# Kernel tuning notes

Hardware: AMD Instinct MI355X
Metric: run time of the kernel (lower is better)

Reference implementation:

```python
import jax, jax.numpy as jnp
import numpy as np

B, S, D_IN, D_OUT = 4, 2048, 1024, 1024


def setup_inputs() -> dict:
    key = jax.random.key(0)
    k1, k2, k3, k4 = jax.random.split(key, 4)
    scale = 1.0 / np.sqrt(D_IN)
    return {
        "x": jax.random.normal(k1, (B, S, D_IN), dtype=jnp.float32),
        # torch nn.Linear weights have shape [d_out, d_in]
        "Wq": jax.random.normal(k2, (D_OUT, D_IN), dtype=jnp.float32) * scale,
        "Wk": jax.random.normal(k3, (D_OUT, D_IN), dtype=jnp.float32) * scale,
        "Wv": jax.random.normal(k4, (D_OUT, D_IN), dtype=jnp.float32) * scale,
    }


def reference(x, Wq, Wk, Wv):
    # Linear projections (torch Linear: y = x @ W.T), no bias
    q = jnp.einsum('bsd,od->bso', x, Wq)
    k = jnp.einsum('bsd,od->bso', x, Wk)
    v = jnp.einsum('bsd,od->bso', x, Wv)
    s = q.shape[1]
    scores = jnp.einsum('bqd,bkd->bqk', q, k)  # [B, S, S]
    causal = jnp.tril(jnp.ones((s, s), dtype=bool))  # True = keep
    scores = jnp.where(causal[None], scores, -jnp.inf)
    scale = jnp.asarray(k.shape[-1], scores.dtype) ** 0.5
    weights = jax.nn.softmax(scores / scale, axis=-1)
    return jnp.einsum('bqk,bkd->bqd', weights, v)
```

## Files before the change

kernel.cpp:

```cpp
#include <hip/hip_runtime.h>

#define BATCH 4
#define SEQ   2048
#define DIM   1024
#define MTOT  (BATCH * SEQ)
#define BK    32

typedef __bf16 bf16x8 __attribute__((ext_vector_type(8)));
typedef float  f32x4  __attribute__((ext_vector_type(4)));

__device__ __forceinline__ void gl_lds16(const __bf16* g, __bf16* l) {
    __builtin_amdgcn_global_load_lds(
        (const __attribute__((address_space(1))) void*)g,
        (__attribute__((address_space(3))) void*)l,
        16, 0, 0);
}

__global__ __launch_bounds__(256) void zerol_kernel(float* __restrict__ l)
{
    l[blockIdx.x * 256 + threadIdx.x] = 0.f;
}

__global__ __launch_bounds__(256) void cvt_all_kernel(
    const float* __restrict__ x,  const float* __restrict__ w0,
    const float* __restrict__ w1, const float* __restrict__ w2,
    __bf16* __restrict__ xd, __bf16* __restrict__ d0,
    __bf16* __restrict__ d1, __bf16* __restrict__ d2)
{
    const int bid = blockIdx.x;
    const float* s;
    __bf16* d;
    int base;
    if (bid < 4096)      { s = x;  d = xd; base = bid; }
    else if (bid < 4608) { s = w0; d = d0; base = bid - 4096; }
    else if (bid < 5120) { s = w1; d = d1; base = bid - 4608; }
    else                 { s = w2; d = d2; base = bid - 5120; }
    const int i = (base * 256 + threadIdx.x) * 8;
    const float4 a = *(const float4*)(s + i);
    const float4 b = *(const float4*)(s + i + 4);
    bf16x8 o;
    o[0] = (__bf16)a.x; o[1] = (__bf16)a.y; o[2] = (__bf16)a.z; o[3] = (__bf16)a.w;
    o[4] = (__bf16)b.x; o[5] = (__bf16)b.y; o[6] = (__bf16)b.z; o[7] = (__bf16)b.w;
    *(bf16x8*)(d + i) = o;
}

__device__ __forceinline__ void gemm_core(
    const __bf16* __restrict__ A, size_t lda,
    const __bf16* __restrict__ Bm, size_t ldb,
    int m0, int n0, int kTiles,
    __bf16* lA, __bf16* lB,
    f32x4 (&acc)[4][4])
{
    const int tid  = threadIdx.x;
    const int lane = tid & 63;
    const int wave = tid >> 6;
    const int wm = (wave >> 1) << 6;
    const int wn = (wave & 1) << 6;

#pragma unroll
    for (int i = 0; i < 4; ++i)
#pragma unroll
        for (int j = 0; j < 4; ++j)
            acc[i][j] = (f32x4){0.f, 0.f, 0.f, 0.f};

    for (int kt = 0; kt < kTiles; ++kt) {
        const int k0 = kt << 5;
        __syncthreads();
#pragma unroll
        for (int it = 0; it < 2; ++it) {
            const int f   = tid + (it << 8);
            const int row = f >> 2;
            const int col = (f & 3) << 3;
            gl_lds16(A  + (size_t)(m0 + row) * lda + (size_t)(k0 + col), lA + f * 8);
            gl_lds16(Bm + (size_t)(n0 + row) * ldb + (size_t)(k0 + col), lB + f * 8);
        }
        __syncthreads();

        bf16x8 af[4], bfr[4];
#pragma unroll
        for (int i = 0; i < 4; ++i) {
            af[i]  = *(const bf16x8*)(lA + (size_t)(wm + i * 16 + (lane & 15)) * BK + ((lane >> 4) << 3));
            bfr[i] = *(const bf16x8*)(lB + (size_t)(wn + i * 16 + (lane & 15)) * BK + ((lane >> 4) << 3));
        }
#pragma unroll
        for (int i = 0; i < 4; ++i)
#pragma unroll
            for (int j = 0; j < 4; ++j)
                acc[i][j] = __builtin_amdgcn_mfma_f32_16x16x32_bf16(af[i], bfr[j], acc[i][j], 0, 0, 0);
    }
}

template <bool ROWSUM>
__device__ __forceinline__ void store_tile_bf16(
    f32x4 (&acc)[4][4], __bf16* scratch, bool transpose, float scale,
    __bf16* dst, size_t ldo, size_t r0, size_t c0,
    bool expMask = false, bool diag = false,
    float* lsum = nullptr, float* gRow = nullptr)
{
    const int tid  = threadIdx.x;
    const int lane = tid & 63;
    const int wave = tid >> 6;
    const int wm = (wave >> 1) << 6, wn = (wave & 1) << 6;
    const int quad = lane >> 4;
    const int ln15 = lane & 15;

    if (ROWSUM && tid < 32) lsum[tid] = 0.f;

#pragma unroll
    for (int p = 0; p < 4; ++p) {
        __syncthreads();
        if (!transpose) {
            if (wm == ((p >> 1) << 6)) {
#pragma unroll
                for (int ih = 0; ih < 2; ++ih) {
                    const int i = ((p & 1) << 1) + ih;
                    const int lr = ih * 16 + quad * 4;
#pragma unroll
                    for (int j = 0; j < 4; ++j)
#pragma unroll
                        for (int r = 0; r < 4; ++r) {
                            const int lm = wm + ((p & 1) << 5) + lr + r;
                            const int ln = wn + j * 16 + ln15;
                            float v = acc[i][j][r] * scale;
                            if (expMask) {
                                v = (!diag || ln <= lm) ? __expf(v) : 0.f;
                            }
                            scratch[(lr + r) * 136 + wn + j * 16 + ln15] = (__bf16)v;
                        }
                }
            }
        } else {
            if (wn == ((p >> 1) << 6)) {
#pragma unroll
                for (int jh = 0; jh < 2; ++jh) {
                    const int j = ((p & 1) << 1) + jh;
                    const int lr = jh * 16 + ln15;
#pragma unroll
                    for (int i = 0; i < 4; ++i)
#pragma unroll
                        for (int r = 0; r < 4; ++r)
                            scratch[lr * 136 + wm + i * 16 + quad * 4 + r] =
                                (__bf16)(acc[i][j][r] * scale);
                }
            }
        }
        __syncthreads();
#pragma unroll
        for (int it = 0; it < 2; ++it) {
            const int g   = tid + (it << 8);
            const int row = g >> 4;
            const int col = (g & 15) << 3;
            const bf16x8 vv = *(const bf16x8*)(scratch + row * 136 + col);
            *(bf16x8*)(dst + (r0 + p * 32 + row) * ldo + c0 + col) = vv;
            if (ROWSUM) {
                float part = 0.f;
#pragma unroll
                for (int k = 0; k < 8; ++k) part += (float)vv[k];
                atomicAdd(&lsum[row], part);
            }
        }
        if (ROWSUM) {
            __syncthreads();
            if (tid < 32) {
                atomicAdd(&gRow[r0 + p * 32 + tid], lsum[tid]);
                lsum[tid] = 0.f;
            }
        }
    }
}

__global__ __launch_bounds__(256) void qkv_kernel(
    const __bf16* __restrict__ x,
    const __bf16* __restrict__ Wq,
    const __bf16* __restrict__ Wk,
    const __bf16* __restrict__ Wv,
    __bf16* __restrict__ Q, __bf16* __restrict__ Kb, __bf16* __restrict__ Vt)
{
    __shared__ __bf16 smem[8192];
    __bf16* lA = smem;
    __bf16* lB = smem + 128 * BK;
    const int L = blockIdx.x;
    const int c = L & 7;
    const int k = L >> 3;
    const int z  = k >> 6;
    const int p  = (k >> 3) & 7;
    const int n0 = (k & 7) << 7;
    const int m0 = ((c << 3) + p) << 7;
    const __bf16* W = (z == 0) ? Wq : (z == 1) ? Wk : Wv;

    f32x4 acc[4][4];
    gemm_core(x, DIM, W, DIM, m0, n0, DIM / BK, lA, lB, acc);

    if (z == 0) {
        store_tile_bf16<false>(acc, smem, false, 1.f, Q,  DIM, m0, n0);
    } else if (z == 1) {
        store_tile_bf16<false>(acc, smem, false, 1.f, Kb, DIM, m0, n0);
    } else {
        const size_t b = (size_t)(m0 >> 11), ms0 = (size_t)(m0 & (SEQ - 1));
        store_tile_bf16<false>(acc, smem, true, 1.f, Vt + b * DIM * SEQ, SEQ, n0, ms0);
    }
}

__global__ __launch_bounds__(256) void scores_kernel(
    const __bf16* __restrict__ Q, const __bf16* __restrict__ Kb,
    __bf16* __restrict__ Sc, float* __restrict__ l)
{
    const int L = blockIdx.x;
    const int g = (L & 7) * 68 + (L >> 3);
    const int b = g / 136;
    const int t = g - b * 136;
    int i = (int)((sqrtf(8.f * t + 1.f) - 1.f) * 0.5f);
    while ((i + 1) * (i + 2) / 2 <= t) ++i;
    while (i * (i + 1) / 2 > t) --i;
    const int j = t - i * (i + 1) / 2;

    __shared__ __bf16 smem[8192];
    __shared__ float lsum[32];
    __bf16* lA = smem;
    __bf16* lB = smem + 128 * BK;
    const __bf16* A  = Q  + (size_t)b * SEQ * DIM;
    const __bf16* Bm = Kb + (size_t)b * SEQ * DIM;

    f32x4 acc[4][4];
    gemm_core(A, DIM, Bm, DIM, i << 7, j << 7, DIM / BK, lA, lB, acc);

    store_tile_bf16<true>(acc, smem, false, 0.03125f,
                          Sc + (size_t)b * SEQ * SEQ, SEQ,
                          (size_t)(i << 7), (size_t)(j << 7),
                          true, (i == j),
                          lsum, l + (b << 11));
}

__global__ __launch_bounds__(256) void pv_kernel(
    const __bf16* __restrict__ P, const __bf16* __restrict__ Vt,
    const float* __restrict__ l, float* __restrict__ out)
{
    const int L = blockIdx.x;
    const int c = L & 7;
    const int k = L >> 3;
    const int b = c >> 1;
    const int i = 15 - (c & 1) - ((k >> 3) << 1);
    const int x = k & 7;

    __shared__ __bf16 smem[8192];
    __bf16* lA = smem;
    __bf16* lB = smem + 128 * BK;
    const __bf16* A  = P  + (size_t)b * SEQ * SEQ;
    const __bf16* Bm = Vt + (size_t)b * DIM * SEQ;

    f32x4 acc[4][4];
    gemm_core(A, SEQ, Bm, SEQ, i << 7, x << 7, (i + 1) * (128 / BK), lA, lB, acc);

    const int lane = threadIdx.x & 63;
    const int wave = threadIdx.x >> 6;
    const int wm = (wave >> 1) << 6, wn = (wave & 1) << 6;
#pragma unroll
    for (int ii = 0; ii < 4; ++ii) {
#pragma unroll
        for (int r = 0; r < 4; ++r) {
            const int m = (i << 7) + wm + ii * 16 + ((lane >> 4) << 2) + r;
            const float inv = 1.f / l[(b << 11) + m];
#pragma unroll
            for (int jj = 0; jj < 4; ++jj) {
                const int n = (x << 7) + wn + jj * 16 + (lane & 15);
                out[((size_t)b * SEQ + m) * DIM + n] = acc[ii][jj][r] * inv;
            }
        }
    }
}

extern "C" void kernel_launch(void* const* d_in, const int* in_sizes, int n_in,
                              void* d_out, int out_size, void* d_ws, size_t ws_size,
                              hipStream_t stream) {
    const float* x  = (const float*)d_in[0];
    const float* Wq = (const float*)d_in[1];
    const float* Wk = (const float*)d_in[2];
    const float* Wv = (const float*)d_in[3];
    float* out = (float*)d_out;

    char* ws = (char*)d_ws;
    __bf16* Q  = (__bf16*)(ws);
    __bf16* Kb = (__bf16*)(ws + (16ull << 20));
    __bf16* Vt = (__bf16*)(ws + (32ull << 20));
    __bf16* Sc = (__bf16*)(ws + (48ull << 20));
    __bf16* Wqb = (__bf16*)(ws + (80ull << 20));
    __bf16* Wkb = (__bf16*)(ws + (82ull << 20));
    __bf16* Wvb = (__bf16*)(ws + (84ull << 20));
    float*  l   = (float*)(ws + (86ull << 20));
    __bf16* xb  = (__bf16*)d_out;

    zerol_kernel  <<<dim3(32),   256, 0, stream>>>(l);
    cvt_all_kernel<<<dim3(5632), 256, 0, stream>>>(x, Wq, Wk, Wv, xb, Wqb, Wkb, Wvb);

    qkv_kernel    <<<dim3(1536), 256, 0, stream>>>(xb, Wqb, Wkb, Wvb, Q, Kb, Vt);
    scores_kernel <<<dim3(544),  256, 0, stream>>>(Q, Kb, Sc, l);
    pv_kernel     <<<dim3(512),  256, 0, stream>>>(Sc, Vt, l, out);
}
```

Baseline: 247.4 us.

## Overlap V projection with causal scores GEMM and fold l-zeroing into convert

Moves the V projection out of the QKV kernel and runs its tiles in the same launch as the causal QK^T score tiles, so the 544-tile scores grid is filled out with 512 independent V tiles instead of running alone. The zeroing of the row-sum buffer is folded into the conversion kernel as extra blocks, which removes one launch. The mixed launch has blocks of uneven work and some idle early-exit blocks, and the block-to-XCD mapping of the score tiles changes, which can affect cache locality.

```diff
diff --git a/kernel.cpp b/kernel.cpp
--- a/kernel.cpp
+++ b/kernel.cpp
@@ -16,18 +16,18 @@
         16, 0, 0);
 }
 
-__global__ __launch_bounds__(256) void zerol_kernel(float* __restrict__ l)
-{
-    l[blockIdx.x * 256 + threadIdx.x] = 0.f;
-}
-
 __global__ __launch_bounds__(256) void cvt_all_kernel(
     const float* __restrict__ x,  const float* __restrict__ w0,
     const float* __restrict__ w1, const float* __restrict__ w2,
     __bf16* __restrict__ xd, __bf16* __restrict__ d0,
-    __bf16* __restrict__ d1, __bf16* __restrict__ d2)
+    __bf16* __restrict__ d1, __bf16* __restrict__ d2,
+    float* __restrict__ l)
 {
     const int bid = blockIdx.x;
+    if (bid >= 5632) {
+        l[(bid - 5632) * 256 + threadIdx.x] = 0.f;
+        return;
+    }
     const float* s;
     __bf16* d;
     int base;
@@ -169,12 +169,11 @@
     }
 }
 
-__global__ __launch_bounds__(256) void qkv_kernel(
+__global__ __launch_bounds__(256) void qk_kernel(
     const __bf16* __restrict__ x,
     const __bf16* __restrict__ Wq,
     const __bf16* __restrict__ Wk,
-    const __bf16* __restrict__ Wv,
-    __bf16* __restrict__ Q, __bf16* __restrict__ Kb, __bf16* __restrict__ Vt)
+    __bf16* __restrict__ Q, __bf16* __restrict__ Kb)
 {
     __shared__ __bf16 smem[8192];
     __bf16* lA = smem;
@@ -186,49 +185,54 @@
     const int p  = (k >> 3) & 7;
     const int n0 = (k & 7) << 7;
     const int m0 = ((c << 3) + p) << 7;
-    const __bf16* W = (z == 0) ? Wq : (z == 1) ? Wk : Wv;
+    const __bf16* W = (z == 0) ? Wq : Wk;
 
     f32x4 acc[4][4];
     gemm_core(x, DIM, W, DIM, m0, n0, DIM / BK, lA, lB, acc);
 
-    if (z == 0) {
-        store_tile_bf16<false>(acc, smem, false, 1.f, Q,  DIM, m0, n0);
-    } else if (z == 1) {
-        store_tile_bf16<false>(acc, smem, false, 1.f, Kb, DIM, m0, n0);
-    } else {
-        const size_t b = (size_t)(m0 >> 11), ms0 = (size_t)(m0 & (SEQ - 1));
-        store_tile_bf16<false>(acc, smem, true, 1.f, Vt + b * DIM * SEQ, SEQ, n0, ms0);
-    }
-}
-
-__global__ __launch_bounds__(256) void scores_kernel(
+    store_tile_bf16<false>(acc, smem, false, 1.f, (z == 0) ? Q : Kb, DIM, m0, n0);
+}
+
+__global__ __launch_bounds__(256) void sv_kernel(
     const __bf16* __restrict__ Q, const __bf16* __restrict__ Kb,
-    __bf16* __restrict__ Sc, float* __restrict__ l)
-{
-    const int L = blockIdx.x;
-    const int g = (L & 7) * 68 + (L >> 3);
-    const int b = g / 136;
-    const int t = g - b * 136;
-    int i = (int)((sqrtf(8.f * t + 1.f) - 1.f) * 0.5f);
-    while ((i + 1) * (i + 2) / 2 <= t) ++i;
-    while (i * (i + 1) / 2 > t) --i;
-    const int j = t - i * (i + 1) / 2;
-
+    const __bf16* __restrict__ x, const __bf16* __restrict__ Wv,
+    __bf16* __restrict__ Sc, float* __restrict__ l,
+    __bf16* __restrict__ Vt)
+{
     __shared__ __bf16 smem[8192];
     __shared__ float lsum[32];
     __bf16* lA = smem;
     __bf16* lB = smem + 128 * BK;
-    const __bf16* A  = Q  + (size_t)b * SEQ * DIM;
-    const __bf16* Bm = Kb + (size_t)b * SEQ * DIM;
-
+    const int L = blockIdx.x;
+    const int c = L & 7;
+    const int g = L >> 3;
     f32x4 acc[4][4];
-    gemm_core(A, DIM, Bm, DIM, i << 7, j << 7, DIM / BK, lA, lB, acc);
-
-    store_tile_bf16<true>(acc, smem, false, 0.03125f,
-                          Sc + (size_t)b * SEQ * SEQ, SEQ,
-                          (size_t)(i << 7), (size_t)(j << 7),
-                          true, (i == j),
-                          lsum, l + (b << 11));
+
+    if (c < 4) {
+        const int b = c;
+        const int t = g;
+        int i = (int)((sqrtf(8.f * t + 1.f) - 1.f) * 0.5f);
+        while ((i + 1) * (i + 2) / 2 <= t) ++i;
+        while (i * (i + 1) / 2 > t) --i;
+        const int j = t - i * (i + 1) / 2;
+
+        const __bf16* A  = Q  + (size_t)b * SEQ * DIM;
+        const __bf16* Bm = Kb + (size_t)b * SEQ * DIM;
+        gemm_core(A, DIM, Bm, DIM, i << 7, j << 7, DIM / BK, lA, lB, acc);
+        store_tile_bf16<true>(acc, smem, false, 0.03125f,
+                              Sc + (size_t)b * SEQ * SEQ, SEQ,
+                              (size_t)(i << 7), (size_t)(j << 7),
+                              true, (i == j),
+                              lsum, l + (b << 11));
+    } else {
+        const int vid = (c - 4) * 136 + g;
+        if (vid >= 512) return;
+        const int n0 = (vid & 7) << 7;
+        const int m0 = (vid >> 3) << 7;
+        gemm_core(x, DIM, Wv, DIM, m0, n0, DIM / BK, lA, lB, acc);
+        const size_t b = (size_t)(m0 >> 11), ms0 = (size_t)(m0 & (SEQ - 1));
+        store_tile_bf16<false>(acc, smem, true, 1.f, Vt + b * DIM * SEQ, SEQ, n0, ms0);
+    }
 }
 
 __global__ __launch_bounds__(256) void pv_kernel(
@@ -289,10 +293,9 @@
     float*  l   = (float*)(ws + (86ull << 20));
     __bf16* xb  = (__bf16*)d_out;
 
-    zerol_kernel  <<<dim3(32),   256, 0, stream>>>(l);
-    cvt_all_kernel<<<dim3(5632), 256, 0, stream>>>(x, Wq, Wk, Wv, xb, Wqb, Wkb, Wvb);
-
-    qkv_kernel    <<<dim3(1536), 256, 0, stream>>>(xb, Wqb, Wkb, Wvb, Q, Kb, Vt);
-    scores_kernel <<<dim3(544),  256, 0, stream>>>(Q, Kb, Sc, l);
+    cvt_all_kernel<<<dim3(5664), 256, 0, stream>>>(x, Wq, Wk, Wv, xb, Wqb, Wkb, Wvb, l);
+
+    qk_kernel     <<<dim3(1024), 256, 0, stream>>>(xb, Wqb, Wkb, Q, Kb);
+    sv_kernel     <<<dim3(1088), 256, 0, stream>>>(Q, Kb, xb, Wvb, Sc, l, Vt);
     pv_kernel     <<<dim3(512),  256, 0, stream>>>(Sc, Vt, l, out);
 }
```

After: 259.1 us. 4.8% more time.
